# Optimization experiments

Measured on AMD Instinct MI355X. Metric: run time of the kernel, lower is better.

Reference implementation:

```python
import jax, jax.numpy as jnp
import numpy as np

# Model constants (match init_kwargs config)
D_MODEL, D_INNER, D_HEAD, N_HEADS = 1024, 2048, 64, 32
D_STATE, D_CONV, CHUNK, N_LAYERS = 64, 4, 256, 2
CONV_DIM = D_INNER + 2 * D_STATE        # n_groups = 1
D_IN_PROJ = 2 * D_INNER + 2 * D_STATE + N_HEADS
B_SZ, L_SEQ = 2, 4096
EPS = 1e-5


def setup_inputs() -> dict:
    key = jax.random.key(0)
    ks = jax.random.split(key, 8)
    x = jax.random.normal(ks[0], (B_SZ, L_SEQ, D_MODEL), jnp.float32)
    in_proj_w = jax.random.normal(ks[1], (N_LAYERS, D_IN_PROJ, D_MODEL), jnp.float32) * 0.02
    conv_w = jax.random.normal(ks[2], (N_LAYERS, CONV_DIM, D_CONV), jnp.float32) * 0.2
    conv_b = jax.random.normal(ks[3], (N_LAYERS, CONV_DIM), jnp.float32) * 0.02
    # dt_bias init as in the torch code: inverse-softplus of dt ~ LogUniform(1e-3, 1e-1)
    dt = jnp.exp(jax.random.uniform(ks[4], (N_LAYERS, N_HEADS))
                 * (np.log(0.1) - np.log(0.001)) + np.log(0.001))
    dt = jnp.clip(dt, 1e-4, None)
    dt_bias = dt + jnp.log(-jnp.expm1(-dt))
    A_log = jnp.log(jax.random.uniform(ks[5], (N_LAYERS, N_HEADS), minval=1.0, maxval=16.0))
    D = jnp.ones((N_LAYERS, N_HEADS), jnp.float32)
    gnorm_w = jnp.ones((N_LAYERS, D_INNER), jnp.float32)
    out_proj_w = jax.random.normal(ks[6], (N_LAYERS, D_MODEL, D_INNER), jnp.float32) * 0.02
    norm_w = jnp.ones((N_LAYERS, D_MODEL), jnp.float32)
    return dict(x=x, in_proj_w=in_proj_w, conv_w=conv_w, conv_b=conv_b, dt_bias=dt_bias,
                A_log=A_log, D=D, gnorm_w=gnorm_w, out_proj_w=out_proj_w, norm_w=norm_w)


def _rmsnorm(x, w, eps=EPS):
    return x * jax.lax.rsqrt(jnp.mean(x * x, axis=-1, keepdims=True) + eps) * w


def _segsum(x):
    # x: (..., T) -> (..., T, T) with S[i, j] = sum_{j < k <= i} x[k], -inf above diag
    T = x.shape[-1]
    cs = jnp.cumsum(x, axis=-1)
    d = cs[..., :, None] - cs[..., None, :]
    return jnp.where(jnp.tril(jnp.ones((T, T), bool)), d, -jnp.inf)


def _causal_conv1d(x, w, b):
    # depthwise causal conv: x (B,L,C), w (C,K), b (C)
    K = w.shape[-1]
    L = x.shape[1]
    xp = jnp.pad(x, ((0, 0), (K - 1, 0), (0, 0)))
    out = jnp.broadcast_to(b, x.shape)
    for i in range(K):
        out = out + xp[:, i:i + L, :] * w[:, i]
    return out


def _ssd(X, dt, A, B, C, D):
    # Exact chunked SSD scan (mamba_chunk_scan_combined), n_groups=1.
    # X (b,l,h,p), dt (b,l,h), A (h), B,C (b,l,n)
    b, l, h, p = X.shape
    n = B.shape[-1]
    nc = l // CHUNK
    Xdt = X * dt[..., None]
    dA = (dt * A).reshape(b, nc, CHUNK, h).transpose(0, 3, 1, 2)     # (b,h,z,c)
    dAcs = jnp.cumsum(dA, axis=-1)
    Lmat = jnp.exp(_segsum(dA))                                      # (b,h,z,c,c)
    Bc = B.reshape(b, nc, CHUNK, n)
    Cc = C.reshape(b, nc, CHUNK, n)
    Xc = Xdt.reshape(b, nc, CHUNK, h, p)
    # intra-chunk (diagonal) part
    G = jnp.einsum('bzln,bzsn->bzls', Cc, Bc)                        # (b,z,c,c)
    M = G[:, None] * Lmat                                            # (b,h,z,c,c)
    Yd = jnp.einsum('bhzls,bzshp->bzlhp', M, Xc)
    # chunk states
    decay_states = jnp.exp(dAcs[..., -1:] - dAcs)                    # (b,h,z,c)
    states = jnp.einsum('bzln,bhzl,bzlhp->bzhpn', Bc, decay_states, Xc)
    # inter-chunk recurrence
    chunk_decay = jnp.exp(_segsum(jnp.pad(dAcs[..., -1], ((0, 0), (0, 0), (1, 0)))))
    states0 = jnp.concatenate([jnp.zeros_like(states[:, :1]), states], axis=1)
    prev = jnp.einsum('bhzc,bchpn->bzhpn', chunk_decay, states0)[:, :-1]
    Yo = jnp.einsum('bzln,bzhpn,bhzl->bzlhp', Cc, prev, jnp.exp(dAcs))
    Y = (Yd + Yo).reshape(b, l, h, p) + X * D[None, None, :, None]
    return Y


def _block(x, in_w, cw, cb, dtb, a_log, d_skip, gw, ow, nw):
    b, l, _ = x.shape
    h = _rmsnorm(x, nw)
    zxbcdt = jnp.einsum('bld,ed->ble', h, in_w)
    z = zxbcdt[..., :D_INNER]
    xBC = zxbcdt[..., D_INNER:D_INNER + CONV_DIM]
    dt = jax.nn.softplus(zxbcdt[..., D_INNER + CONV_DIM:] + dtb)      # (b,l,H)
    xBC = jax.nn.silu(_causal_conv1d(xBC, cw, cb))
    xs = xBC[..., :D_INNER].reshape(b, l, N_HEADS, D_HEAD)
    Bm = xBC[..., D_INNER:D_INNER + D_STATE]
    Cm = xBC[..., D_INNER + D_STATE:]
    A = -jnp.exp(a_log)
    y = _ssd(xs, dt, A, Bm, Cm, d_skip).reshape(b, l, D_INNER)
    y = _rmsnorm(y * jax.nn.silu(z), gw)                              # gated RMSNorm (gate before norm)
    return x + jnp.einsum('bli,di->bld', y, ow)


def reference(x, in_proj_w, conv_w, conv_b, dt_bias, A_log, D, gnorm_w, out_proj_w, norm_w):
    for i in range(in_proj_w.shape[0]):
        x = _block(x, in_proj_w[i], conv_w[i], conv_b[i], dt_bias[i],
                   A_log[i], D[i], gnorm_w[i], out_proj_w[i], norm_w[i])
    return x
```

## Files before the change

kernel.cpp:

```cpp
#include <hip/hip_runtime.h>

#define DMODEL   1024
#define DINNER   2048
#define NHEADS   32
#define DHEAD    64
#define DSTATE   64
#define CONVDIM  2176
#define DINPROJ  4256
#define LSEQ     4096
#define BSZ      2
#define NCHUNK   16
#define CHUNK    256
#define NROWS    8192
#define NPAD     4352
#define XT_P     264
#define M_P      40

typedef __attribute__((ext_vector_type(8))) short  short8;
typedef __attribute__((ext_vector_type(4))) float  f32x4;
typedef __attribute__((ext_vector_type(4))) unsigned short us4;

__device__ __forceinline__ float bf2f(unsigned short u){
  return __uint_as_float(((unsigned int)u) << 16);
}
__device__ __forceinline__ unsigned short f2bf(float f){
  unsigned int i = __float_as_uint(f);
  i += 0x7fffu + ((i >> 16) & 1u);
  return (unsigned short)(i >> 16);
}

__device__ __forceinline__ void gl_lds16(const void* g, void* l){
  __builtin_amdgcn_global_load_lds(
      (const __attribute__((address_space(1))) unsigned int*)g,
      (__attribute__((address_space(3))) unsigned int*)l, 16, 0, 0);
}

__global__ void cast_pad_kernel(const float* __restrict__ src, unsigned short* __restrict__ dst,
                                int rows_src, int cols, long long total){
  long long i = (long long)blockIdx.x * 256 + threadIdx.x;
  if (i >= total) return;
  long long r = i / cols;
  dst[i] = (r < rows_src) ? f2bf(src[i]) : (unsigned short)0;
}

__global__ void rmsnorm_kernel(const float* __restrict__ x, const float* __restrict__ w,
                               unsigned short* __restrict__ out){
  int r = blockIdx.x, t = threadIdx.x;
  const float* xr = x + (size_t)r * DMODEL;
  float v[4]; float s = 0.f;
#pragma unroll
  for (int i = 0; i < 4; ++i){ v[i] = xr[t + i*256]; s += v[i]*v[i]; }
  __shared__ float red[4];
  for (int off = 32; off; off >>= 1) s += __shfl_down(s, off, 64);
  if ((t & 63) == 0) red[t >> 6] = s;
  __syncthreads();
  s = red[0] + red[1] + red[2] + red[3];
  float sc = rsqrtf(s * (1.f/DMODEL) + 1e-5f);
#pragma unroll
  for (int i = 0; i < 4; ++i)
    out[(size_t)r*DMODEL + t + i*256] = f2bf(v[i]*sc*w[t + i*256]);
}

template<int EPI>
__launch_bounds__(256, 3)
__global__ void gemm_bt(const unsigned short* __restrict__ A, const unsigned short* __restrict__ Bw,
                        void* __restrict__ Cout, const float* __restrict__ Cres,
                        int K, int Nstore, int nbx){
  __shared__ __align__(16) unsigned short As[128*64];
  __shared__ __align__(16) unsigned short Bs[128*64];
  int id = blockIdx.x;
  const int nwg = gridDim.x;
  if ((nwg & 7) == 0) id = (id & 7)*(nwg >> 3) + (id >> 3);
  const int m0 = (id / nbx) * 128, n0 = (id % nbx) * 128;
  const int t = threadIdx.x, w = t >> 6, lane = t & 63;
  const int wr = w >> 1, wc = w & 1;
  const int srow = lane >> 3;
  const int scol = (lane & 7) * 8;
  f32x4 acc[4][4] = {};

  for (int k0 = 0; k0 < K; k0 += 64){
#pragma unroll
    for (int it = 0; it < 4; ++it){
      int rr = (w*4 + it)*8 + srow;
      gl_lds16(A  + (size_t)(m0 + rr)*K + k0 + scol, &As[(w*4 + it)*512]);
      gl_lds16(Bw + (size_t)(n0 + rr)*K + k0 + scol, &Bs[(w*4 + it)*512]);
    }
    __syncthreads();
#pragma unroll
    for (int kk = 0; kk < 64; kk += 32){
      short8 af[4], bfr[4];
      int col = kk + (lane >> 4)*8;
#pragma unroll
      for (int m = 0; m < 4; ++m)
        af[m] = *(const short8*)&As[(wr*64 + m*16 + (lane & 15))*64 + col];
#pragma unroll
      for (int n = 0; n < 4; ++n)
        bfr[n] = *(const short8*)&Bs[(wc*64 + n*16 + (lane & 15))*64 + col];
#pragma unroll
      for (int m = 0; m < 4; ++m)
#pragma unroll
        for (int n = 0; n < 4; ++n)
          acc[m][n] = __builtin_amdgcn_mfma_f32_16x16x32_bf16(af[m], bfr[n], acc[m][n], 0, 0, 0);
    }
    __syncthreads();
  }

#pragma unroll
  for (int m = 0; m < 4; ++m){
#pragma unroll
    for (int n = 0; n < 4; ++n){
      int col = n0 + wc*64 + n*16 + (lane & 15);
      if (col < Nstore){
#pragma unroll
        for (int r = 0; r < 4; ++r){
          int row = m0 + wr*64 + m*16 + (lane >> 4)*4 + r;
          if (EPI == 0)
            ((unsigned short*)Cout)[(size_t)row*Nstore + col] = f2bf(acc[m][n][r]);
          else
            ((float*)Cout)[(size_t)row*Nstore + col] =
                Cres[(size_t)row*Nstore + col] + acc[m][n][r];
        }
      }
    }
  }
}

__global__ void conv_silu_kernel(const unsigned short* __restrict__ zx,
                                 const float* __restrict__ cw, const float* __restrict__ cb,
                                 unsigned short* __restrict__ X, unsigned short* __restrict__ Bm,
                                 unsigned short* __restrict__ Cm){
  int gid = blockIdx.x*256 + threadIdx.x;
  if (gid >= (CONVDIM/8)*(NROWS/64)) return;
  const int oc = gid % (CONVDIM/8);
  const int rb = gid / (CONVDIM/8);
  const int c = oc*8;
  const size_t r0 = (size_t)rb*64;
  const int l0 = (int)(r0 & (LSEQ-1));
  float w[4][8], bias[8];
#pragma unroll
  for (int j = 0; j < 8; ++j){
    bias[j] = cb[c+j];
#pragma unroll
    for (int i = 0; i < 4; ++i) w[i][j] = cw[(c+j)*4 + i];
  }
  const unsigned short* src = zx + DINNER + c;
  float p[3][8];
#pragma unroll
  for (int i = 0; i < 3; ++i){
    if (l0 - 3 + i >= 0){
      short8 v = *(const short8*)(src + (r0 - 3 + i)*DINPROJ);
#pragma unroll
      for (int j = 0; j < 8; ++j) p[i][j] = bf2f((unsigned short)v[j]);
    } else {
#pragma unroll
      for (int j = 0; j < 8; ++j) p[i][j] = 0.f;
    }
  }
  for (int it = 0; it < 64; ++it){
    const size_t r = r0 + it;
    short8 v = *(const short8*)(src + r*DINPROJ);
    float cur[8];
    short8 ov;
#pragma unroll
    for (int j = 0; j < 8; ++j){
      cur[j] = bf2f((unsigned short)v[j]);
      float a = bias[j] + w[0][j]*p[0][j] + w[1][j]*p[1][j] + w[2][j]*p[2][j] + w[3][j]*cur[j];
      float s = a / (1.f + __expf(-a));
      ov[j] = (short)f2bf(s);
    }
    if (c < DINNER)             *(short8*)(X  + r*DINNER + c) = ov;
    else if (c < DINNER+DSTATE) *(short8*)(Bm + r*DSTATE + (c-DINNER)) = ov;
    else                        *(short8*)(Cm + r*DSTATE + (c-DINNER-DSTATE)) = ov;
#pragma unroll
    for (int j = 0; j < 8; ++j){ p[0][j]=p[1][j]; p[1][j]=p[2][j]; p[2][j]=cur[j]; }
  }
}

__global__ void dtscan_kernel(const unsigned short* __restrict__ zx, const float* __restrict__ dtb,
                              const float* __restrict__ A_log,
                              float* __restrict__ dt_sp, float* __restrict__ dAcs_g){
  const int z = blockIdx.x, hh = blockIdx.y, b = blockIdx.z;
  const int t = threadIdx.x;
  __shared__ float sdA[CHUNK];
  const float Ah = -__expf(A_log[hh]);
  size_t r = (size_t)b*LSEQ + z*CHUNK + t;
  float raw = bf2f(zx[r*DINPROJ + DINNER + CONVDIM + hh]) + dtb[hh];
  float dtv = raw > 20.f ? raw : log1pf(__expf(raw));
  sdA[t] = dtv * Ah;
  __syncthreads();
  for (int off = 1; off < CHUNK; off <<= 1){
    float v = (t >= off) ? sdA[t - off] : 0.f;
    __syncthreads();
    sdA[t] += v;
    __syncthreads();
  }
  size_t hb = (size_t)(b*NHEADS + hh);
  dt_sp[hb*LSEQ + z*CHUNK + t] = dtv;
  dAcs_g[(hb*NCHUNK + z)*CHUNK + t] = sdA[t];
}

__launch_bounds__(256, 2)
__global__ void chunk_main_kernel(const unsigned short* __restrict__ X,
                                  const unsigned short* __restrict__ Bm,
                                  const unsigned short* __restrict__ Cm,
                                  const float* __restrict__ dt_sp,
                                  const float* __restrict__ dAcs_g,
                                  float* __restrict__ states,
                                  unsigned short* __restrict__ Yb){
  const int z = blockIdx.x, hh = blockIdx.y, b = blockIdx.z;
  const int t = threadIdx.x, w = t >> 6, lane = t & 63;
  __shared__ __align__(16) unsigned short Xt[64 * XT_P];
  __shared__ __align__(16) unsigned short U[64 * XT_P];
  __shared__ float sdA[CHUNK];
  __shared__ float sdt[CHUNK];

  const size_t row0 = (size_t)b*LSEQ + z*CHUNK;
  const size_t hb = (size_t)(b*NHEADS + hh);
  sdA[t] = dAcs_g[(hb*NCHUNK + z)*CHUNK + t];
  sdt[t] = dt_sp[hb*LSEQ + z*CHUNK + t];
  __syncthreads();
  const float total = sdA[CHUNK-1];

  for (int it = 0; it < 16; ++it){
    int l = it*16 + (t >> 4);
    int p4 = (t & 15) * 4;
    float dtl = sdt[l];
    float dec = __expf(total - sdA[l]);
    us4 xv = *(const us4*)(X  + (row0 + l)*DINNER + hh*DHEAD + p4);
    us4 bv = *(const us4*)(Bm + (row0 + l)*DSTATE + p4);
#pragma unroll
    for (int j = 0; j < 4; ++j){
      Xt[(p4 + j)*XT_P + l] = f2bf(bf2f(xv[j]) * dtl);
      U [(p4 + j)*XT_P + l] = f2bf(bf2f(bv[j]) * dec);
    }
  }
  __syncthreads();

  {
    f32x4 sacc[4] = {};
    for (int k2 = 0; k2 < 8; ++k2){
      int kc = k2*32 + (lane >> 4)*8;
      short8 a = *(const short8*)&U[(w*16 + (lane & 15))*XT_P + kc];
#pragma unroll
      for (int pt = 0; pt < 4; ++pt){
        short8 bfr = *(const short8*)&Xt[(pt*16 + (lane & 15))*XT_P + kc];
        sacc[pt] = __builtin_amdgcn_mfma_f32_16x16x32_bf16(a, bfr, sacc[pt], 0, 0, 0);
      }
    }
    float* sp = states + (((size_t)b*NCHUNK + z)*NHEADS + hh)*(DHEAD*DSTATE);
#pragma unroll
    for (int pt = 0; pt < 4; ++pt){
      int p = pt*16 + (lane & 15);
#pragma unroll
      for (int r = 0; r < 4; ++r){
        int n = w*16 + (lane >> 4)*4 + r;
        sp[p*DSTATE + n] = sacc[pt][r];
      }
    }
  }
  __syncthreads();

  unsigned short* Mw = U + w * (64 * M_P);
  short8 cfr[4][2];
#pragma unroll
  for (int lt = 0; lt < 4; ++lt){
    int lg = w + lt*4;
#pragma unroll
    for (int k2 = 0; k2 < 2; ++k2)
      cfr[lt][k2] = *(const short8*)(Cm + (row0 + lg*16 + (lane & 15))*DSTATE + k2*32 + (lane >> 4)*8);
  }
  f32x4 yacc[4][4] = {};
  for (int st = 0; st < 8; ++st){
    short8 gb[2][2];
#pragma unroll
    for (int ss = 0; ss < 2; ++ss)
#pragma unroll
      for (int k2 = 0; k2 < 2; ++k2)
        gb[ss][k2] = *(const short8*)(Bm + (row0 + st*32 + ss*16 + (lane & 15))*DSTATE + k2*32 + (lane >> 4)*8);
    short8 xb[4];
#pragma unroll
    for (int pt = 0; pt < 4; ++pt)
      xb[pt] = *(const short8*)&Xt[(pt*16 + (lane & 15))*XT_P + st*32 + (lane >> 4)*8];
#pragma unroll
    for (int lt = 0; lt < 4; ++lt){
      int lg = w + lt*4;
      if (st*32 > lg*16 + 15) continue;
#pragma unroll
      for (int ss = 0; ss < 2; ++ss){
        f32x4 g = {};
        g = __builtin_amdgcn_mfma_f32_16x16x32_bf16(cfr[lt][0], gb[ss][0], g, 0, 0, 0);
        g = __builtin_amdgcn_mfma_f32_16x16x32_bf16(cfr[lt][1], gb[ss][1], g, 0, 0, 0);
        int s = st*32 + ss*16 + (lane & 15);
        float sdAs = sdA[s];
#pragma unroll
        for (int r = 0; r < 4; ++r){
          int l = lg*16 + (lane >> 4)*4 + r;
          float m = (s <= l) ? __expf(sdA[l] - sdAs) : 0.f;
          Mw[(lt*16 + (lane >> 4)*4 + r)*M_P + ss*16 + (lane & 15)] = f2bf(g[r] * m);
        }
      }
      short8 mf = *(const short8*)&Mw[(lt*16 + (lane & 15))*M_P + (lane >> 4)*8];
#pragma unroll
      for (int pt = 0; pt < 4; ++pt)
        yacc[lt][pt] = __builtin_amdgcn_mfma_f32_16x16x32_bf16(mf, xb[pt], yacc[lt][pt], 0, 0, 0);
    }
  }
  __syncthreads();

  unsigned short* Yst = U + w * 4096;
#pragma unroll
  for (int lt = 0; lt < 4; ++lt)
#pragma unroll
    for (int pt = 0; pt < 4; ++pt)
#pragma unroll
      for (int r = 0; r < 4; ++r){
        int row = lt*16 + (lane >> 4)*4 + r;
        int c = pt*16 + (lane & 15);
        int cs = (c & 7) | ((((c >> 3) ^ (row & 7)) & 7) << 3);
        Yst[row*64 + cs] = f2bf(yacc[lt][pt][r]);
      }
  __syncthreads();
  {
    int ltl = lane >> 4, rr = lane & 15;
    int row = ltl*16 + rr;
    int lg = (w + ltl*4)*16 + rr;
    unsigned short* dst = Yb + (row0 + lg)*DINNER + hh*DHEAD;
#pragma unroll
    for (int k = 0; k < 8; ++k){
      short8 v = *(const short8*)&Yst[row*64 + ((k ^ (row & 7)) << 3)];
      *(short8*)(dst + k*8) = v;
    }
  }
}

__launch_bounds__(256)
__global__ void state_recur_kernel(const float* __restrict__ states, const float* __restrict__ dAcs_g,
                                   unsigned short* __restrict__ prev_bf){
  const int hh = blockIdx.x, b = blockIdx.y, t = threadIdx.x;
  float S[16];
#pragma unroll
  for (int k = 0; k < 16; ++k) S[k] = 0.f;
  for (int z = 0; z < NCHUNK; ++z){
    size_t base = (((size_t)b*NCHUNK + z)*NHEADS + hh)*(DHEAD*DSTATE);
    float cd = __expf(dAcs_g[(((size_t)(b*NHEADS + hh))*NCHUNK + z)*CHUNK + CHUNK-1]);
#pragma unroll
    for (int k = 0; k < 16; ++k){
      size_t idx = base + (size_t)k*256 + t;
      float st = states[idx];
      prev_bf[idx] = f2bf(S[k]);
      S[k] = S[k]*cd + st;
    }
  }
}

__launch_bounds__(512, 2)
__global__ void chunk_fin_kernel(const unsigned short* __restrict__ X,
                                 const unsigned short* __restrict__ Cm,
                                 const unsigned short* __restrict__ zx,
                                 const float* __restrict__ dAcs_g,
                                 const unsigned short* __restrict__ prev_bf,
                                 const float* __restrict__ Dp,
                                 const unsigned short* __restrict__ Yb,
                                 const float* __restrict__ gnw,
                                 unsigned short* __restrict__ yn){
  const int s = blockIdx.x;
  const int b = blockIdx.y;
  const int z = s >> 4, sl = s & 15;
  const int t = threadIdx.x, w = t >> 6, lane = t & 63;
  const size_t row0 = (size_t)b*LSEQ + z*CHUNK + sl*16;
  __shared__ __align__(16) unsigned short Yg[16][2056];
  __shared__ float seA[NHEADS][16];
  __shared__ float sDp[NHEADS];

  {
    int hh = t >> 4, r = t & 15;
    seA[hh][r] = __expf(dAcs_g[(((size_t)(b*NHEADS + hh))*NCHUNK + z)*CHUNK + sl*16 + r]);
    if (t < NHEADS) sDp[t] = Dp[t];
  }
  __syncthreads();

  short8 cf[2];
#pragma unroll
  for (int k2 = 0; k2 < 2; ++k2)
    cf[k2] = *(const short8*)(Cm + (row0 + (lane & 15))*DSTATE + k2*32 + (lane >> 4)*8);

  for (int hi = 0; hi < 4; ++hi){
    int hh = w*4 + hi;
    const unsigned short* pvb = prev_bf + (((size_t)b*NCHUNK + z)*NHEADS + hh)*(DHEAD*DSTATE);
    f32x4 acc[4] = {};
#pragma unroll
    for (int k2 = 0; k2 < 2; ++k2){
      int kc = k2*32 + (lane >> 4)*8;
#pragma unroll
      for (int pt = 0; pt < 4; ++pt){
        short8 bv = *(const short8*)(pvb + (size_t)(pt*16 + (lane & 15))*DSTATE + kc);
        acc[pt] = __builtin_amdgcn_mfma_f32_16x16x32_bf16(cf[k2], bv, acc[pt], 0, 0, 0);
      }
    }
#pragma unroll
    for (int pt = 0; pt < 4; ++pt){
      int c = hh*DHEAD + pt*16 + (lane & 15);
#pragma unroll
      for (int r = 0; r < 4; ++r){
        int row = (lane >> 4)*4 + r;
        Yg[row][c] = f2bf(acc[pt][r] * seA[hh][row]);
      }
    }
  }
  __syncthreads();

  const int row = t >> 5, i = t & 31;
  const size_t grow = row0 + row;
  float ss = 0.f;
#pragma unroll
  for (int j = 0; j < 8; ++j){
    int c0 = i*8 + j*256;
    short8 yo = *(const short8*)&Yg[row][c0];
    short8 yd = *(const short8*)(Yb + grow*DINNER + c0);
    short8 xv = *(const short8*)(X  + grow*DINNER + c0);
    short8 zv = *(const short8*)(zx + grow*DINPROJ + c0);
    float Dh = sDp[c0 >> 6];
    short8 og;
#pragma unroll
    for (int q = 0; q < 8; ++q){
      float y = bf2f((unsigned short)yd[q]) + bf2f((unsigned short)yo[q])
              + Dh*bf2f((unsigned short)xv[q]);
      float zf = bf2f((unsigned short)zv[q]);
      float g = y * (zf / (1.f + __expf(-zf)));
      ss += g*g;
      og[q] = (short)f2bf(g);
    }
    *(short8*)&Yg[row][c0] = og;
  }
  for (int off = 16; off; off >>= 1) ss += __shfl_down(ss, off, 32);
  float sc = __shfl(ss, 0, 32);
  sc = rsqrtf(sc * (1.f/DINNER) + 1e-5f);
  __syncthreads();

#pragma unroll
  for (int j = 0; j < 8; ++j){
    int c0 = i*8 + j*256;
    short8 g = *(const short8*)&Yg[row][c0];
    f32x4 w0 = *(const f32x4*)(gnw + c0);
    f32x4 w1 = *(const f32x4*)(gnw + c0 + 4);
    short8 o;
#pragma unroll
    for (int q = 0; q < 4; ++q) o[q]   = (short)f2bf(bf2f((unsigned short)g[q])  *sc*w0[q]);
#pragma unroll
    for (int q = 0; q < 4; ++q) o[q+4] = (short)f2bf(bf2f((unsigned short)g[q+4])*sc*w1[q]);
    *(short8*)(yn + grow*DINNER + c0) = o;
  }
}

extern "C" void kernel_launch(void* const* d_in, const int* in_sizes, int n_in,
                              void* d_out, int out_size, void* d_ws, size_t ws_size,
                              hipStream_t stream){
  const float* x      = (const float*)d_in[0];
  const float* in_w   = (const float*)d_in[1];
  const float* conv_w = (const float*)d_in[2];
  const float* conv_b = (const float*)d_in[3];
  const float* dt_b   = (const float*)d_in[4];
  const float* A_log  = (const float*)d_in[5];
  const float* Dp     = (const float*)d_in[6];
  const float* gnw    = (const float*)d_in[7];
  const float* out_w  = (const float*)d_in[8];
  const float* norm_w = (const float*)d_in[9];
  float* outp = (float*)d_out;

  const size_t NEEDED =
      (size_t)NROWS*DMODEL*2 + (size_t)NPAD*DMODEL*2 + (size_t)DMODEL*DINNER*2
    + (size_t)NROWS*DINPROJ*2 + (size_t)NROWS*DINNER*2  + (size_t)NROWS*DINNER*2
    + (size_t)NROWS*DSTATE*2*2 + (size_t)BSZ*NHEADS*LSEQ*4
    + (size_t)BSZ*NHEADS*NCHUNK*CHUNK*4
    + (size_t)BSZ*NCHUNK*NHEADS*DHEAD*DSTATE*4
    + (size_t)BSZ*NCHUNK*NHEADS*DHEAD*DSTATE*2
    + 40*256;
  if (ws_size < NEEDED) return;

  char* p = (char*)d_ws;
  auto alloc = [&](size_t n){ char* r = p; p += (n + 255) & ~(size_t)255; return (void*)r; };
  unsigned short* h    = (unsigned short*)alloc((size_t)NROWS*DMODEL*2);
  unsigned short* wA   = (unsigned short*)alloc((size_t)NPAD*DMODEL*2);
  unsigned short* wO   = (unsigned short*)alloc((size_t)DMODEL*DINNER*2);
  unsigned short* zx   = (unsigned short*)alloc((size_t)NROWS*DINPROJ*2);
  unsigned short* X    = (unsigned short*)alloc((size_t)NROWS*DINNER*2);
  unsigned short* Yb   = (unsigned short*)alloc((size_t)NROWS*DINNER*2);
  unsigned short* Bm   = (unsigned short*)alloc((size_t)NROWS*DSTATE*2);
  unsigned short* Cm   = (unsigned short*)alloc((size_t)NROWS*DSTATE*2);
  float* dtbuf  = (float*)alloc((size_t)BSZ*NHEADS*LSEQ*4);
  float* dAcs   = (float*)alloc((size_t)BSZ*NHEADS*NCHUNK*CHUNK*4);
  float* states = (float*)alloc((size_t)BSZ*NCHUNK*NHEADS*DHEAD*DSTATE*4);
  unsigned short* prev_bf = (unsigned short*)alloc((size_t)BSZ*NCHUNK*NHEADS*DHEAD*DSTATE*2);
  unsigned short* yn = X;

  for (int layer = 0; layer < 2; ++layer){
    const float* xprev = (layer == 0) ? x : outp;
    float* xnext = outp;

    cast_pad_kernel<<<(NPAD*DMODEL + 255)/256, 256, 0, stream>>>(
        in_w + (size_t)layer*DINPROJ*DMODEL, wA, DINPROJ, DMODEL, (long long)NPAD*DMODEL);
    rmsnorm_kernel<<<NROWS, 256, 0, stream>>>(xprev, norm_w + layer*DMODEL, h);
    gemm_bt<0><<<dim3((NPAD/128)*(NROWS/128)), 256, 0, stream>>>(
        h, wA, (void*)zx, nullptr, DMODEL, DINPROJ, NPAD/128);
    conv_silu_kernel<<<((CONVDIM/8)*(NROWS/64) + 255)/256, 256, 0, stream>>>(
        zx, conv_w + (size_t)layer*CONVDIM*4, conv_b + layer*CONVDIM, X, Bm, Cm);
    dtscan_kernel<<<dim3(NCHUNK, NHEADS, BSZ), 256, 0, stream>>>(
        zx, dt_b + layer*NHEADS, A_log + layer*NHEADS, dtbuf, dAcs);
    chunk_main_kernel<<<dim3(NCHUNK, NHEADS, BSZ), 256, 0, stream>>>(
        X, Bm, Cm, dtbuf, dAcs, states, Yb);
    state_recur_kernel<<<dim3(NHEADS, BSZ), 256, 0, stream>>>(states, dAcs, prev_bf);
    chunk_fin_kernel<<<dim3(256, BSZ), 512, 0, stream>>>(
        X, Cm, zx, dAcs, prev_bf, Dp + layer*NHEADS, Yb, gnw + (size_t)layer*DINNER, yn);
    cast_pad_kernel<<<(DMODEL*DINNER + 255)/256, 256, 0, stream>>>(
        out_w + (size_t)layer*DMODEL*DINNER, wO, DMODEL, DINNER, (long long)DMODEL*DINNER);
    gemm_bt<1><<<dim3((DMODEL/128)*(NROWS/128)), 256, 0, stream>>>(
        yn, wO, (void*)xnext, xprev, DINNER, DMODEL, DMODEL/128);
  }
  (void)in_sizes; (void)n_in; (void)out_size;
}
```

Measured before the change: 696.7 us.

## Use double-buffered 256x256 swizzled GEMM tile for the in-projection

Adds a new GEMM kernel for the in-projection that uses 256x256 tiles with 512 threads, double-buffered LDS staging that overlaps the next tile's global loads with MFMA compute, an XOR-swizzled LDS layout to avoid bank conflicts, and setprio around the MFMA burst. The larger tile is meant to raise data reuse per loaded byte and hide load latency. It also drops the block-id remapping from the original 128-tile GEMM, which is still used for the out-projection. The trade-off is one block per CU with high register and LDS use, and only 32x17 = 544 blocks, which leaves less room for latency hiding through occupancy and gives a somewhat uneven final wave.

```diff
diff --git a/kernel.cpp b/kernel.cpp
--- a/kernel.cpp
+++ b/kernel.cpp
@@ -62,15 +62,95 @@
 }
 
 template<int EPI>
+__launch_bounds__(512, 1)
+__global__ void gemm256_bt(const unsigned short* __restrict__ A, const unsigned short* __restrict__ Bw,
+                           void* __restrict__ Cout, const float* __restrict__ Cres,
+                           int K, int Nstore, int nbx){
+  __shared__ __align__(16) unsigned short As[2][256*64];
+  __shared__ __align__(16) unsigned short Bs[2][256*64];
+  const int id = blockIdx.x;
+  const int m0 = (id / nbx) * 256, n0 = (id % nbx) * 256;
+  const int t = threadIdx.x, w = t >> 6, lane = t & 63;
+  const int wr = w >> 2, wc = w & 3;
+  const int nt = K >> 6;
+  const int swz = ((lane & 7) ^ (lane >> 3)) * 8;
+
+  auto STAGE = [&](int slot, int tile){
+    const int k0 = tile << 6;
+#pragma unroll
+    for (int i = 0; i < 4; ++i){
+      int rA = i*64 + w*8 + (lane >> 3);
+      gl_lds16(A  + (size_t)(m0 + rA)*K + k0 + swz, &As[slot][i*4096 + w*512]);
+      gl_lds16(Bw + (size_t)(n0 + rA)*K + k0 + swz, &Bs[slot][i*4096 + w*512]);
+    }
+  };
+
+  f32x4 acc[8][4] = {};
+  STAGE(0, 0);
+  for (int tt = 0; tt < nt; ++tt){
+    if (tt + 1 < nt){
+      STAGE((tt+1)&1, tt+1);
+      asm volatile("s_waitcnt vmcnt(8)" ::: "memory");
+    } else {
+      asm volatile("s_waitcnt vmcnt(0)" ::: "memory");
+    }
+    __builtin_amdgcn_s_barrier();
+    const unsigned short* Ab = As[tt&1];
+    const unsigned short* Bb = Bs[tt&1];
+#pragma unroll
+    for (int k2 = 0; k2 < 2; ++k2){
+      short8 af[8], bv[4];
+      const int slot = k2*4 + (lane >> 4);
+#pragma unroll
+      for (int mf = 0; mf < 8; ++mf){
+        int row = wr*128 + mf*16 + (lane & 15);
+        af[mf] = *(const short8*)&Ab[row*64 + ((slot ^ (row & 7)) * 8)];
+      }
+#pragma unroll
+      for (int nf = 0; nf < 4; ++nf){
+        int row = wc*64 + nf*16 + (lane & 15);
+        bv[nf] = *(const short8*)&Bb[row*64 + ((slot ^ (row & 7)) * 8)];
+      }
+      __builtin_amdgcn_s_setprio(1);
+#pragma unroll
+      for (int mf = 0; mf < 8; ++mf)
+#pragma unroll
+        for (int nf = 0; nf < 4; ++nf)
+          acc[mf][nf] = __builtin_amdgcn_mfma_f32_16x16x32_bf16(af[mf], bv[nf], acc[mf][nf], 0, 0, 0);
+      __builtin_amdgcn_s_setprio(0);
+    }
+    asm volatile("s_waitcnt lgkmcnt(0)" ::: "memory");
+    __builtin_amdgcn_s_barrier();
+  }
+
+#pragma unroll
+  for (int mf = 0; mf < 8; ++mf){
+#pragma unroll
+    for (int nf = 0; nf < 4; ++nf){
+      int col = n0 + wc*64 + nf*16 + (lane & 15);
+      if (col < Nstore){
+#pragma unroll
+        for (int r = 0; r < 4; ++r){
+          int row = m0 + wr*128 + mf*16 + (lane >> 4)*4 + r;
+          if (EPI == 0)
+            ((unsigned short*)Cout)[(size_t)row*Nstore + col] = f2bf(acc[mf][nf][r]);
+          else
+            ((float*)Cout)[(size_t)row*Nstore + col] =
+                Cres[(size_t)row*Nstore + col] + acc[mf][nf][r];
+        }
+      }
+    }
+  }
+}
+
+template<int EPI>
 __launch_bounds__(256, 3)
 __global__ void gemm_bt(const unsigned short* __restrict__ A, const unsigned short* __restrict__ Bw,
                         void* __restrict__ Cout, const float* __restrict__ Cres,
                         int K, int Nstore, int nbx){
   __shared__ __align__(16) unsigned short As[128*64];
   __shared__ __align__(16) unsigned short Bs[128*64];
-  int id = blockIdx.x;
-  const int nwg = gridDim.x;
-  if ((nwg & 7) == 0) id = (id & 7)*(nwg >> 3) + (id >> 3);
+  const int id = blockIdx.x;
   const int m0 = (id / nbx) * 128, n0 = (id % nbx) * 128;
   const int t = threadIdx.x, w = t >> 6, lane = t & 63;
   const int wr = w >> 1, wc = w & 1;
@@ -500,8 +580,8 @@
     cast_pad_kernel<<<(NPAD*DMODEL + 255)/256, 256, 0, stream>>>(
         in_w + (size_t)layer*DINPROJ*DMODEL, wA, DINPROJ, DMODEL, (long long)NPAD*DMODEL);
     rmsnorm_kernel<<<NROWS, 256, 0, stream>>>(xprev, norm_w + layer*DMODEL, h);
-    gemm_bt<0><<<dim3((NPAD/128)*(NROWS/128)), 256, 0, stream>>>(
-        h, wA, (void*)zx, nullptr, DMODEL, DINPROJ, NPAD/128);
+    gemm256_bt<0><<<dim3((NROWS/256)*(NPAD/256)), 512, 0, stream>>>(
+        h, wA, (void*)zx, nullptr, DMODEL, DINPROJ, NPAD/256);
     conv_silu_kernel<<<((CONVDIM/8)*(NROWS/64) + 255)/256, 256, 0, stream>>>(
         zx, conv_w + (size_t)layer*CONVDIM*4, conv_b + layer*CONVDIM, X, Bm, Cm);
     dtscan_kernel<<<dim3(NCHUNK, NHEADS, BSZ), 256, 0, stream>>>(
```

Result: slower. 715.3 us (+2.7%).

## Precompute head-shared C·Bᵀ Gram matrix once per chunk instead of per head

Applied to the files above, without the earlier changes.

Since B and C are shared across all heads (one group), a new gram_kernel computes the 256x256 C·Bᵀ matrix per chunk once and stores it in bf16; chunk_main then reads it and applies the per-head decay mask in registers, removing 32x redundant MFMA work and the LDS round-trip for the masked matrix. It adds a global buffer and an extra launch, and double-rounds G to bf16. Separately, the GEMM grid is changed to a 2D launch, dropping the XCD-aware block-index swizzle, which may change L2 locality.

```diff
diff --git a/kernel.cpp b/kernel.cpp
--- a/kernel.cpp
+++ b/kernel.cpp
@@ -14,7 +14,6 @@
 #define NROWS    8192
 #define NPAD     4352
 #define XT_P     264
-#define M_P      40
 
 typedef __attribute__((ext_vector_type(8))) short  short8;
 typedef __attribute__((ext_vector_type(4))) float  f32x4;
@@ -65,13 +64,10 @@
 __launch_bounds__(256, 3)
 __global__ void gemm_bt(const unsigned short* __restrict__ A, const unsigned short* __restrict__ Bw,
                         void* __restrict__ Cout, const float* __restrict__ Cres,
-                        int K, int Nstore, int nbx){
+                        int K, int Nstore){
   __shared__ __align__(16) unsigned short As[128*64];
   __shared__ __align__(16) unsigned short Bs[128*64];
-  int id = blockIdx.x;
-  const int nwg = gridDim.x;
-  if ((nwg & 7) == 0) id = (id & 7)*(nwg >> 3) + (id >> 3);
-  const int m0 = (id / nbx) * 128, n0 = (id % nbx) * 128;
+  const int m0 = blockIdx.y * 128, n0 = blockIdx.x * 128;
   const int t = threadIdx.x, w = t >> 6, lane = t & 63;
   const int wr = w >> 1, wc = w & 1;
   const int srow = lane >> 3;
@@ -199,10 +195,48 @@
   dAcs_g[(hb*NCHUNK + z)*CHUNK + t] = sdA[t];
 }
 
+__launch_bounds__(256, 4)
+__global__ void gram_kernel(const unsigned short* __restrict__ Bm,
+                            const unsigned short* __restrict__ Cm,
+                            unsigned short* __restrict__ Gb){
+  const int zq = blockIdx.x, b = blockIdx.y;
+  const int z = zq >> 2, rq = zq & 3;
+  const int t = threadIdx.x, w = t >> 6, lane = t & 63;
+  const size_t row0 = (size_t)b*LSEQ + z*CHUNK;
+  f32x4 acc[4][4] = {};
+#pragma unroll
+  for (int k2 = 0; k2 < 2; ++k2){
+    int kc = k2*32 + (lane >> 4)*8;
+    short8 cf[4], bfr[4];
+#pragma unroll
+    for (int mf = 0; mf < 4; ++mf)
+      cf[mf] = *(const short8*)(Cm + (row0 + rq*64 + mf*16 + (lane & 15))*DSTATE + kc);
+#pragma unroll
+    for (int nf = 0; nf < 4; ++nf)
+      bfr[nf] = *(const short8*)(Bm + (row0 + w*64 + nf*16 + (lane & 15))*DSTATE + kc);
+#pragma unroll
+    for (int mf = 0; mf < 4; ++mf)
+#pragma unroll
+      for (int nf = 0; nf < 4; ++nf)
+        acc[mf][nf] = __builtin_amdgcn_mfma_f32_16x16x32_bf16(cf[mf], bfr[nf], acc[mf][nf], 0, 0, 0);
+  }
+  unsigned short* Gp = Gb + (((size_t)b*NCHUNK + z) << 16);
+#pragma unroll
+  for (int mf = 0; mf < 4; ++mf)
+#pragma unroll
+    for (int nf = 0; nf < 4; ++nf)
+#pragma unroll
+      for (int r = 0; r < 4; ++r){
+        int row = rq*64 + mf*16 + (lane >> 4)*4 + r;
+        int col = w*64 + nf*16 + (lane & 15);
+        Gp[(size_t)row*256 + col] = f2bf(acc[mf][nf][r]);
+      }
+}
+
 __launch_bounds__(256, 2)
 __global__ void chunk_main_kernel(const unsigned short* __restrict__ X,
                                   const unsigned short* __restrict__ Bm,
-                                  const unsigned short* __restrict__ Cm,
+                                  const unsigned short* __restrict__ Gb,
                                   const float* __restrict__ dt_sp,
                                   const float* __restrict__ dAcs_g,
                                   float* __restrict__ states,
@@ -260,46 +294,30 @@
   }
   __syncthreads();
 
-  unsigned short* Mw = U + w * (64 * M_P);
-  short8 cfr[4][2];
-#pragma unroll
-  for (int lt = 0; lt < 4; ++lt){
-    int lg = w + lt*4;
-#pragma unroll
-    for (int k2 = 0; k2 < 2; ++k2)
-      cfr[lt][k2] = *(const short8*)(Cm + (row0 + lg*16 + (lane & 15))*DSTATE + k2*32 + (lane >> 4)*8);
-  }
+  const unsigned short* Gp = Gb + (((size_t)b*NCHUNK + z) << 16);
   f32x4 yacc[4][4] = {};
   for (int st = 0; st < 8; ++st){
-    short8 gb[2][2];
-#pragma unroll
-    for (int ss = 0; ss < 2; ++ss)
-#pragma unroll
-      for (int k2 = 0; k2 < 2; ++k2)
-        gb[ss][k2] = *(const short8*)(Bm + (row0 + st*32 + ss*16 + (lane & 15))*DSTATE + k2*32 + (lane >> 4)*8);
     short8 xb[4];
 #pragma unroll
     for (int pt = 0; pt < 4; ++pt)
       xb[pt] = *(const short8*)&Xt[(pt*16 + (lane & 15))*XT_P + st*32 + (lane >> 4)*8];
+    const int s0 = st*32 + (lane >> 4)*8;
+    float es[8];
+#pragma unroll
+    for (int j = 0; j < 8; ++j) es[j] = sdA[s0 + j];
 #pragma unroll
     for (int lt = 0; lt < 4; ++lt){
       int lg = w + lt*4;
       if (st*32 > lg*16 + 15) continue;
-#pragma unroll
-      for (int ss = 0; ss < 2; ++ss){
-        f32x4 g = {};
-        g = __builtin_amdgcn_mfma_f32_16x16x32_bf16(cfr[lt][0], gb[ss][0], g, 0, 0, 0);
-        g = __builtin_amdgcn_mfma_f32_16x16x32_bf16(cfr[lt][1], gb[ss][1], g, 0, 0, 0);
-        int s = st*32 + ss*16 + (lane & 15);
-        float sdAs = sdA[s];
-#pragma unroll
-        for (int r = 0; r < 4; ++r){
-          int l = lg*16 + (lane >> 4)*4 + r;
-          float m = (s <= l) ? __expf(sdA[l] - sdAs) : 0.f;
-          Mw[(lt*16 + (lane >> 4)*4 + r)*M_P + ss*16 + (lane & 15)] = f2bf(g[r] * m);
-        }
-      }
-      short8 mf = *(const short8*)&Mw[(lt*16 + (lane & 15))*M_P + (lane >> 4)*8];
+      int l = lg*16 + (lane & 15);
+      float el = sdA[l];
+      short8 gv = *(const short8*)&Gp[(size_t)l*256 + s0];
+      short8 mf;
+#pragma unroll
+      for (int j = 0; j < 8; ++j){
+        float m = (s0 + j <= l) ? bf2f((unsigned short)gv[j]) * __expf(el - es[j]) : 0.f;
+        mf[j] = (short)f2bf(m);
+      }
 #pragma unroll
       for (int pt = 0; pt < 4; ++pt)
         yacc[lt][pt] = __builtin_amdgcn_mfma_f32_16x16x32_bf16(mf, xb[pt], yacc[lt][pt], 0, 0, 0);
@@ -474,7 +492,8 @@
     + (size_t)BSZ*NHEADS*NCHUNK*CHUNK*4
     + (size_t)BSZ*NCHUNK*NHEADS*DHEAD*DSTATE*4
     + (size_t)BSZ*NCHUNK*NHEADS*DHEAD*DSTATE*2
-    + 40*256;
+    + (size_t)BSZ*NCHUNK*CHUNK*CHUNK*2
+    + 48*256;
   if (ws_size < NEEDED) return;
 
   char* p = (char*)d_ws;
@@ -491,6 +510,7 @@
   float* dAcs   = (float*)alloc((size_t)BSZ*NHEADS*NCHUNK*CHUNK*4);
   float* states = (float*)alloc((size_t)BSZ*NCHUNK*NHEADS*DHEAD*DSTATE*4);
   unsigned short* prev_bf = (unsigned short*)alloc((size_t)BSZ*NCHUNK*NHEADS*DHEAD*DSTATE*2);
+  unsigned short* Gb = (unsigned short*)alloc((size_t)BSZ*NCHUNK*CHUNK*CHUNK*2);
   unsigned short* yn = X;
 
   for (int layer = 0; layer < 2; ++layer){
@@ -500,21 +520,22 @@
     cast_pad_kernel<<<(NPAD*DMODEL + 255)/256, 256, 0, stream>>>(
         in_w + (size_t)layer*DINPROJ*DMODEL, wA, DINPROJ, DMODEL, (long long)NPAD*DMODEL);
     rmsnorm_kernel<<<NROWS, 256, 0, stream>>>(xprev, norm_w + layer*DMODEL, h);
-    gemm_bt<0><<<dim3((NPAD/128)*(NROWS/128)), 256, 0, stream>>>(
-        h, wA, (void*)zx, nullptr, DMODEL, DINPROJ, NPAD/128);
+    gemm_bt<0><<<dim3(NPAD/128, NROWS/128), 256, 0, stream>>>(
+        h, wA, (void*)zx, nullptr, DMODEL, DINPROJ);
     conv_silu_kernel<<<((CONVDIM/8)*(NROWS/64) + 255)/256, 256, 0, stream>>>(
         zx, conv_w + (size_t)layer*CONVDIM*4, conv_b + layer*CONVDIM, X, Bm, Cm);
     dtscan_kernel<<<dim3(NCHUNK, NHEADS, BSZ), 256, 0, stream>>>(
         zx, dt_b + layer*NHEADS, A_log + layer*NHEADS, dtbuf, dAcs);
+    gram_kernel<<<dim3(NCHUNK*4, BSZ), 256, 0, stream>>>(Bm, Cm, Gb);
     chunk_main_kernel<<<dim3(NCHUNK, NHEADS, BSZ), 256, 0, stream>>>(
-        X, Bm, Cm, dtbuf, dAcs, states, Yb);
+        X, Bm, Gb, dtbuf, dAcs, states, Yb);
     state_recur_kernel<<<dim3(NHEADS, BSZ), 256, 0, stream>>>(states, dAcs, prev_bf);
     chunk_fin_kernel<<<dim3(256, BSZ), 512, 0, stream>>>(
         X, Cm, zx, dAcs, prev_bf, Dp + layer*NHEADS, Yb, gnw + (size_t)layer*DINNER, yn);
     cast_pad_kernel<<<(DMODEL*DINNER + 255)/256, 256, 0, stream>>>(
         out_w + (size_t)layer*DMODEL*DINNER, wO, DMODEL, DINNER, (long long)DMODEL*DINNER);
-    gemm_bt<1><<<dim3((DMODEL/128)*(NROWS/128)), 256, 0, stream>>>(
-        yn, wO, (void*)xnext, xprev, DINNER, DMODEL, DMODEL/128);
+    gemm_bt<1><<<dim3(DMODEL/128, NROWS/128), 256, 0, stream>>>(
+        yn, wO, (void*)xnext, xprev, DINNER, DMODEL);
   }
   (void)in_sizes; (void)n_in; (void)out_size;
 }
```

Result: no change. 683.2 us (-1.9%).
